# Optimization experiments

Measured on AMD Instinct MI355X. Metric: run time of the kernel, lower is better.

Reference implementation:

```python
import jax, jax.numpy as jnp
import numpy as np

INTERVAL_A = 0
INTERVAL_B = 255  # interval = [a, b]
T = 1_000_000

def setup_inputs() -> dict:
    key = jax.random.key(0)
    signal = jax.random.normal(key, (T,), dtype=jnp.float32)
    return {"signal": signal}

def reference(signal):
    # Always (globally) operator over interval [a, b] with padding='last':
    # out[t] = min_{i in [t+a, t+b]} padded_signal[i]
    # This is exactly equivalent to the original tril/triu masked T x T
    # matrix followed by a hard min along the time axis (Minish with
    # because every window [t+a, t+b] is non-empty within the padded signal.
    a, b = INTERVAL_A, INTERVAL_B
    Tn = signal.shape[0]
    pad_value = signal[-1]  # padding='last'
    padded = jnp.concatenate([signal, jnp.full((b + 1,), pad_value, signal.dtype)])  # [T + b + 1]
    # gather windows: [T, b-a+1]
    idx = jnp.arange(Tn)[:, None] + jnp.arange(a, b + 1)[None, :]
    windows = padded[idx]
    return jnp.min(windows, axis=1)  # [T]
```

## Files before the change

kernel.cpp:

```cpp
#include <hip/hip_runtime.h>

#define W 256

__global__ __launch_bounds__(W) void slidemin_kernel(const float* __restrict__ sig,
                                                     float* __restrict__ out,
                                                     int T) {
    __shared__ float s[2 * W];
    const int t = threadIdx.x;
    const int base = blockIdx.x * W;
    const int g0 = base + t;
    const int g1 = g0 + W;

    s[t]     = sig[g0 < T ? g0 : T - 1];
    s[W + t] = sig[g1 < T ? g1 : T - 1];
    __syncthreads();

    #pragma unroll
    for (int off = 1; off < W; off <<= 1) {
        float a = s[t];
        float b = (t + off < W) ? s[t + off] : a;
        float c = s[W + t];
        float d = (t >= off) ? s[W + t - off] : c;
        __syncthreads();
        s[t]     = fminf(a, b);
        s[W + t] = fminf(c, d);
        __syncthreads();
    }

    if (g0 < T) {
        float v = (t == 0) ? s[0] : fminf(s[t], s[W + t - 1]);
        out[g0] = v;
    }
}

extern "C" void kernel_launch(void* const* d_in, const int* in_sizes, int n_in,
                              void* d_out, int out_size, void* d_ws, size_t ws_size,
                              hipStream_t stream) {
    const float* sig = (const float*)d_in[0];
    float* out = (float*)d_out;
    const int T = in_sizes[0];
    const int nblk = (T + W - 1) / W;
    slidemin_kernel<<<nblk, W, 0, stream>>>(sig, out, T);
}
```

Before: 11.38 us.

## Compute sliding-window min per wavefront with register scans and shuffles

Replaces the block-wide shared-memory Hillis-Steele suffix/prefix scans with one wavefront per 256-element segment. Each lane loads four elements as float4, does serial local scans in registers, then runs wave-level shuffle scans, which removes LDS traffic and the __syncthreads barriers. The trade is more shuffle instructions and a dependence on the 64-lane wavefront width.

```diff
diff --git a/kernel.cpp b/kernel.cpp
--- a/kernel.cpp
+++ b/kernel.cpp
@@ -1,35 +1,85 @@
 #include <hip/hip_runtime.h>
+#include <math.h>
 
-#define W 256
+#define SEG 256
+#define WAVES_PER_BLOCK 4
+#define BLOCK (WAVES_PER_BLOCK * 64)
 
-__global__ __launch_bounds__(W) void slidemin_kernel(const float* __restrict__ sig,
-                                                     float* __restrict__ out,
-                                                     int T) {
-    __shared__ float s[2 * W];
-    const int t = threadIdx.x;
-    const int base = blockIdx.x * W;
-    const int g0 = base + t;
-    const int g1 = g0 + W;
+__global__ __launch_bounds__(BLOCK) void slidemin_wave(const float* __restrict__ sig,
+                                                       float* __restrict__ out,
+                                                       int T, int nseg) {
+    const int lane = threadIdx.x & 63;
+    const int wid  = threadIdx.x >> 6;
+    const int seg  = blockIdx.x * WAVES_PER_BLOCK + wid;
+    if (seg >= nseg) return;
 
-    s[t]     = sig[g0 < T ? g0 : T - 1];
-    s[W + t] = sig[g1 < T ? g1 : T - 1];
-    __syncthreads();
+    const int base = seg * SEG;
+    const int g0 = base + lane * 4;
+    const int g1 = g0 + SEG;
 
-    #pragma unroll
-    for (int off = 1; off < W; off <<= 1) {
-        float a = s[t];
-        float b = (t + off < W) ? s[t + off] : a;
-        float c = s[W + t];
-        float d = (t >= off) ? s[W + t - off] : c;
-        __syncthreads();
-        s[t]     = fminf(a, b);
-        s[W + t] = fminf(c, d);
-        __syncthreads();
+    float a0, a1, a2, a3, b0, b1, b2, b3;
+    if (g1 + 3 < T) {
+        float4 va = *reinterpret_cast<const float4*>(sig + g0);
+        float4 vb = *reinterpret_cast<const float4*>(sig + g1);
+        a0 = va.x; a1 = va.y; a2 = va.z; a3 = va.w;
+        b0 = vb.x; b1 = vb.y; b2 = vb.z; b3 = vb.w;
+    } else {
+        const int tm1 = T - 1;
+        a0 = sig[g0 + 0 < T ? g0 + 0 : tm1];
+        a1 = sig[g0 + 1 < T ? g0 + 1 : tm1];
+        a2 = sig[g0 + 2 < T ? g0 + 2 : tm1];
+        a3 = sig[g0 + 3 < T ? g0 + 3 : tm1];
+        b0 = sig[g1 + 0 < T ? g1 + 0 : tm1];
+        b1 = sig[g1 + 1 < T ? g1 + 1 : tm1];
+        b2 = sig[g1 + 2 < T ? g1 + 2 : tm1];
+        b3 = sig[g1 + 3 < T ? g1 + 3 : tm1];
     }
 
-    if (g0 < T) {
-        float v = (t == 0) ? s[0] : fminf(s[t], s[W + t - 1]);
-        out[g0] = v;
+    float ls3 = a3;
+    float ls2 = fminf(a2, ls3);
+    float ls1 = fminf(a1, ls2);
+    float ls0 = fminf(a0, ls1);
+    float lp0 = b0;
+    float lp1 = fminf(lp0, b1);
+    float lp2 = fminf(lp1, b2);
+    float lp3 = fminf(lp2, b3);
+
+    float A = ls0;
+    #pragma unroll
+    for (int off = 1; off < 64; off <<= 1) {
+        float u = __shfl_down(A, off, 64);
+        if (lane + off < 64) A = fminf(A, u);
+    }
+    float sExcl = __shfl_down(A, 1, 64);
+    if (lane == 63) sExcl = INFINITY;
+
+    float B = lp3;
+    #pragma unroll
+    for (int off = 1; off < 64; off <<= 1) {
+        float u = __shfl_up(B, off, 64);
+        if (lane >= off) B = fminf(B, u);
+    }
+    float pExcl = __shfl_up(B, 1, 64);
+    if (lane == 0) pExcl = INFINITY;
+
+    float s0 = fminf(ls0, sExcl);
+    float s1 = fminf(ls1, sExcl);
+    float s2 = fminf(ls2, sExcl);
+    float s3 = fminf(ls3, sExcl);
+
+    float4 o;
+    o.x = fminf(s0, pExcl);
+    o.y = fminf(s1, fminf(pExcl, lp0));
+    o.z = fminf(s2, fminf(pExcl, lp1));
+    o.w = fminf(s3, fminf(pExcl, lp2));
+
+    if (g0 + 3 < T) {
+        *reinterpret_cast<float4*>(out + g0) = o;
+    } else {
+        if (g0 + 0 < T) out[g0 + 0] = o.x;
+        if (g0 + 1 < T) out[g0 + 1] = o.y;
+        if (g0 + 2 < T) out[g0 + 2] = o.z;
+        if (g0 + 3 < T) out[g0 + 3] = o.w;
     }
 }
 
@@ -39,6 +89,7 @@
     const float* sig = (const float*)d_in[0];
     float* out = (float*)d_out;
     const int T = in_sizes[0];
-    const int nblk = (T + W - 1) / W;
-    slidemin_kernel<<<nblk, W, 0, stream>>>(sig, out, T);
+    const int nseg = (T + SEG - 1) / SEG;
+    const int nblk = (nseg + WAVES_PER_BLOCK - 1) / WAVES_PER_BLOCK;
+    slidemin_wave<<<nblk, BLOCK, 0, stream>>>(sig, out, T, nseg);
 }
```

Result: faster. 10.09 us (-11.3%).
